# Kernel optimization log

Measured on AMD Instinct MI355X. Metric: run time of the kernel, lower is better.

Reference implementation:

```python
import jax, jax.numpy as jnp
import numpy as np

T, B, D, H, L = 64, 512, 1536, 1024, 4
DISCOUNT = 0.997
LAM = 0.95


def setup_inputs() -> dict:
    key = jax.random.key(0)
    ks = jax.random.split(key, 3 + L + 1)
    inp = {
        'feat': jax.random.normal(ks[0], (T, B, D), dtype=jnp.float32),
        'reward': jax.random.normal(ks[1], (T - 1, B), dtype=jnp.float32),
        'cont': jnp.ones((T, B), dtype=jnp.float32),
    }
    scale = 0.02
    dims = [D] + [H] * L
    for i in range(L):
        inp[f'W{i}'] = jax.random.normal(ks[3 + i], (dims[i], dims[i + 1]), dtype=jnp.float32) * scale
        inp[f'b{i}'] = jnp.zeros((dims[i + 1],), dtype=jnp.float32)
    inp['Wo'] = jax.random.normal(ks[3 + L], (H,), dtype=jnp.float32) * scale
    inp['bo'] = jnp.zeros((), dtype=jnp.float32)
    return inp


def reference(feat, reward, cont, W0, b0, W1, b1, W2, b2, W3, b3, Wo, bo):
    # Value-net MLP (mean of critic dist): [T, B, D] -> [T, B]
    h = feat
    for W, b in ((W0, b0), (W1, b1), (W2, b2), (W3, b3)):
        h = jax.nn.silu(h @ W + b)
    value = h @ Wo + bo  # [T, B]

    disc = cont[1:] * DISCOUNT                      # [T-1, B]
    deltas = reward + disc * value[1:] - value[:-1]  # [T-1, B]

    # GAE: adv_t = delta_t + disc_t * lambda * adv_{t+1}, adv_T = 0
    def step(adv_next, xs):
        delta, dl = xs
        adv = delta + dl * adv_next
        return adv, adv

    _, advs = jax.lax.scan(step, jnp.zeros_like(value[0]),
                           (deltas, disc * LAM), reverse=True)
    ret = advs + value[:-1]   # lambda-return target, [T-1, B]
    baseline = value[:-1]
    return ret, baseline
```

## Files before the change

kernel.cpp:

```cpp
#include <hip/hip_runtime.h>
#include <hip/hip_bf16.h>

#define T_DIM 64
#define B_DIM 512
#define D_DIM 1536
#define H_DIM 1024
#define M_DIM (T_DIM * B_DIM)
#define DISCOUNT 0.997f
#define LAM 0.95f

#define BM 128
#define BN 128
#define BK 64
#define TILES_M 256
#define TILES_N 8
#define N_XCD 8

typedef __bf16 bf16x8 __attribute__((ext_vector_type(8)));
typedef float  f32x4  __attribute__((ext_vector_type(4)));

__device__ __forceinline__ void async_load16(const void* g, void* l) {
    __builtin_amdgcn_global_load_lds(
        (const __attribute__((address_space(1))) void*)g,
        (__attribute__((address_space(3))) void*)l,
        16, 0, 0);
}

__device__ __forceinline__ unsigned short f2bf_raw(float f) {
    __hip_bfloat16 h = __float2bfloat16(f);
    return *reinterpret_cast<unsigned short*>(&h);
}

__global__ __launch_bounds__(256) void cvt_bf16_kernel(
    const float* __restrict__ x, __hip_bfloat16* __restrict__ y, long n4) {
    long i = (long)blockIdx.x * blockDim.x + threadIdx.x;
    if (i >= n4) return;
    float4 v = reinterpret_cast<const float4*>(x)[i];
    ushort4 o;
    o.x = f2bf_raw(v.x);
    o.y = f2bf_raw(v.y);
    o.z = f2bf_raw(v.z);
    o.w = f2bf_raw(v.w);
    reinterpret_cast<ushort4*>(y)[i] = o;
}

__global__ __launch_bounds__(256) void transpose_cvt_all_kernel(
    const float* __restrict__ W0, const float* __restrict__ W1,
    const float* __restrict__ W2, const float* __restrict__ W3,
    __hip_bfloat16* __restrict__ T0, __hip_bfloat16* __restrict__ T1,
    __hip_bfloat16* __restrict__ T2, __hip_bfloat16* __restrict__ T3) {
    __shared__ float tile[32][33];
    int z = blockIdx.z;
    const float* W;
    __hip_bfloat16* Tt;
    int K;
    if (z == 0)      { W = W0; Tt = T0; K = D_DIM; }
    else if (z == 1) { W = W1; Tt = T1; K = H_DIM; }
    else if (z == 2) { W = W2; Tt = T2; K = H_DIM; }
    else             { W = W3; Tt = T3; K = H_DIM; }
    int k0 = blockIdx.x * 32, n0 = blockIdx.y * 32;
    if (k0 >= K) return;
    int tx = threadIdx.x, ty = threadIdx.y;
    #pragma unroll
    for (int r = ty; r < 32; r += 8)
        tile[r][tx] = W[(size_t)(k0 + r) * H_DIM + n0 + tx];
    __syncthreads();
    #pragma unroll
    for (int r = ty; r < 32; r += 8)
        Tt[(size_t)(n0 + r) * K + k0 + tx] = __float2bfloat16(tile[tx][r]);
}

__global__ __launch_bounds__(256) void gemm_silu_kernel(
    const __hip_bfloat16* __restrict__ A,
    const __hip_bfloat16* __restrict__ Bt,
    const float* __restrict__ bias,
    __hip_bfloat16* __restrict__ C,
    int K) {

    __shared__ alignas(16) __hip_bfloat16 As[2][BM * BK];
    __shared__ alignas(16) __hip_bfloat16 Bs[2][BN * BK];

    const int tid  = threadIdx.x;
    const int wave = tid >> 6;
    const int lane = tid & 63;
    const int sub  = lane >> 3;
    const int quad = lane >> 4;
    const int r16  = lane & 15;
    const int wm   = wave & 1;
    const int wn   = wave >> 1;

    const int l     = blockIdx.x;
    const int xcd   = l & (N_XCD - 1);
    const int local = l >> 3;
    const int tn    = local & (TILES_N - 1);
    const int tm    = (xcd << 5) | (local >> 3);
    const int m0 = tm * BM;
    const int n0 = tn * BN;

    const int scol = (((lane & 7) ^ sub) << 3);

    const __hip_bfloat16* ga[4];
    const __hip_bfloat16* gb[4];
    int ldsoff[4];
    #pragma unroll
    for (int i = 0; i < 4; ++i) {
        int chunk = wave * 4 + i;
        ga[i] = A  + (size_t)(m0 + chunk * 8 + sub) * K + scol;
        gb[i] = Bt + (size_t)(n0 + chunk * 8 + sub) * K + scol;
        ldsoff[i] = chunk * 512;
    }

    f32x4 acc[4][4];
    #pragma unroll
    for (int i = 0; i < 4; ++i)
        #pragma unroll
        for (int j = 0; j < 4; ++j)
            acc[i][j] = (f32x4){0.f, 0.f, 0.f, 0.f};

    const int niter = K / BK;

    #pragma unroll
    for (int i = 0; i < 4; ++i) { async_load16(ga[i], &As[0][ldsoff[i]]); ga[i] += BK; }
    #pragma unroll
    for (int i = 0; i < 4; ++i) { async_load16(gb[i], &Bs[0][ldsoff[i]]); gb[i] += BK; }

    int p = 0;
    for (int k = 0; k < niter; ++k) {
        asm volatile("s_waitcnt vmcnt(0)" ::: "memory");
        asm volatile("s_barrier" ::: "memory");

        if (k + 1 < niter) {
            #pragma unroll
            for (int i = 0; i < 4; ++i) { async_load16(ga[i], &As[p ^ 1][ldsoff[i]]); ga[i] += BK; }
            #pragma unroll
            for (int i = 0; i < 4; ++i) { async_load16(gb[i], &Bs[p ^ 1][ldsoff[i]]); gb[i] += BK; }
        }

        #pragma unroll
        for (int kk = 0; kk < BK; kk += 32) {
            bf16x8 af[4], bf[4];
            #pragma unroll
            for (int i = 0; i < 4; ++i) {
                int m_l = wm * 64 + i * 16 + r16;
                int sa  = ((kk >> 3) + quad) ^ (m_l & 7);
                af[i] = *reinterpret_cast<const bf16x8*>(&As[p][m_l * BK + sa * 8]);
                int n_l = wn * 64 + i * 16 + r16;
                int sb  = ((kk >> 3) + quad) ^ (n_l & 7);
                bf[i] = *reinterpret_cast<const bf16x8*>(&Bs[p][n_l * BK + sb * 8]);
            }
            #pragma unroll
            for (int i = 0; i < 4; ++i)
                #pragma unroll
                for (int j = 0; j < 4; ++j)
                    acc[i][j] = __builtin_amdgcn_mfma_f32_16x16x32_bf16(
                        af[i], bf[j], acc[i][j], 0, 0, 0);
        }
        p ^= 1;
    }

    #pragma unroll
    for (int j = 0; j < 4; ++j) {
        int col = n0 + wn * 64 + j * 16 + r16;
        float bj = bias[col];
        #pragma unroll
        for (int i = 0; i < 4; ++i) {
            int row_base = m0 + wm * 64 + i * 16 + quad * 4;
            #pragma unroll
            for (int rr = 0; rr < 4; ++rr) {
                float v = acc[i][j][rr] + bj;
                float s = v / (1.f + __expf(-v));
                C[(size_t)(row_base + rr) * H_DIM + col] = __float2bfloat16(s);
            }
        }
    }
}

__global__ __launch_bounds__(256) void gemv_value_kernel(
    const __hip_bfloat16* __restrict__ H,
    const float* __restrict__ Wo,
    const float* __restrict__ bo_p,
    float* __restrict__ value, int M) {
    int wave = threadIdx.x >> 6, lane = threadIdx.x & 63;
    int row = blockIdx.x * 4 + wave;
    if (row >= M) return;
    const __hip_bfloat16* hrow = H + (size_t)row * H_DIM;
    float sum = 0.f;
    #pragma unroll
    for (int half = 0; half < 2; ++half) {
        int col = half * 512 + lane * 8;
        uint4 raw = *reinterpret_cast<const uint4*>(hrow + col);
        const __hip_bfloat16* hp = reinterpret_cast<const __hip_bfloat16*>(&raw);
        #pragma unroll
        for (int e = 0; e < 8; ++e)
            sum += __bfloat162float(hp[e]) * Wo[col + e];
    }
    #pragma unroll
    for (int off = 32; off > 0; off >>= 1)
        sum += __shfl_down(sum, off, 64);
    if (lane == 0) value[row] = sum + bo_p[0];
}

__global__ __launch_bounds__(64) void gae_kernel(
    const float* __restrict__ value,
    const float* __restrict__ reward,
    const float* __restrict__ cont,
    float* __restrict__ out) {
    int b = blockIdx.x * blockDim.x + threadIdx.x;
    if (b >= B_DIM) return;
    float adv = 0.f;
    float v_next = value[(T_DIM - 1) * B_DIM + b];
    for (int t = T_DIM - 2; t >= 0; --t) {
        float v_t  = value[t * B_DIM + b];
        float disc = cont[(t + 1) * B_DIM + b] * DISCOUNT;
        float delta = reward[t * B_DIM + b] + disc * v_next - v_t;
        adv = delta + disc * LAM * adv;
        out[t * B_DIM + b] = adv + v_t;
        out[(T_DIM - 1) * B_DIM + t * B_DIM + b] = v_t;
        v_next = v_t;
    }
}

extern "C" void kernel_launch(void* const* d_in, const int* in_sizes, int n_in,
                              void* d_out, int out_size, void* d_ws, size_t ws_size,
                              hipStream_t stream) {
    const float* feat   = (const float*)d_in[0];
    const float* reward = (const float*)d_in[1];
    const float* cont   = (const float*)d_in[2];
    const float* W[4]   = {(const float*)d_in[3], (const float*)d_in[5],
                           (const float*)d_in[7], (const float*)d_in[9]};
    const float* bias[4] = {(const float*)d_in[4], (const float*)d_in[6],
                            (const float*)d_in[8], (const float*)d_in[10]};
    const float* Wo = (const float*)d_in[11];
    const float* bo = (const float*)d_in[12];
    float* out = (float*)d_out;

    char* ws = (char*)d_ws;
    __hip_bfloat16* Xb = (__hip_bfloat16*)ws; ws += (size_t)M_DIM * D_DIM * 2;
    __hip_bfloat16* Ha = (__hip_bfloat16*)ws; ws += (size_t)M_DIM * H_DIM * 2;
    __hip_bfloat16* Hb = (__hip_bfloat16*)ws; ws += (size_t)M_DIM * H_DIM * 2;
    __hip_bfloat16* Wt0 = (__hip_bfloat16*)ws; ws += (size_t)H_DIM * D_DIM * 2;
    __hip_bfloat16* Wt1 = (__hip_bfloat16*)ws; ws += (size_t)H_DIM * H_DIM * 2;
    __hip_bfloat16* Wt2 = (__hip_bfloat16*)ws; ws += (size_t)H_DIM * H_DIM * 2;
    __hip_bfloat16* Wt3 = (__hip_bfloat16*)ws; ws += (size_t)H_DIM * H_DIM * 2;
    float* value = (float*)ws; ws += (size_t)M_DIM * 4;

    long n4 = (long)M_DIM * D_DIM / 4;
    cvt_bf16_kernel<<<(int)((n4 + 255) / 256), 256, 0, stream>>>(feat, Xb, n4);

    transpose_cvt_all_kernel<<<dim3(D_DIM / 32, H_DIM / 32, 4), dim3(32, 8), 0, stream>>>(
        W[0], W[1], W[2], W[3], Wt0, Wt1, Wt2, Wt3);

    const int nblocks = TILES_M * TILES_N;
    gemm_silu_kernel<<<nblocks, 256, 0, stream>>>(Xb, Wt0, bias[0], Ha, D_DIM);
    gemm_silu_kernel<<<nblocks, 256, 0, stream>>>(Ha, Wt1, bias[1], Hb, H_DIM);
    gemm_silu_kernel<<<nblocks, 256, 0, stream>>>(Hb, Wt2, bias[2], Ha, H_DIM);
    gemm_silu_kernel<<<nblocks, 256, 0, stream>>>(Ha, Wt3, bias[3], Hb, H_DIM);

    gemv_value_kernel<<<M_DIM / 4, 256, 0, stream>>>(Hb, Wo, bo, value, M_DIM);

    gae_kernel<<<8, 64, 0, stream>>>(value, reward, cont, out);
}
```

Measured before the change: 758.3 us.

## Enlarge GEMM tiles to 256x256 and fuse value GEMV into last layer

Each GEMM block now computes a 256x256 tile with 512 threads, using dynamic LDS for the double-buffered A/B tiles. Each wave holds an 8x4 grid of MFMA accumulators, which raises operand reuse per LDS read and halves global re-reads of A and B. The final layer skips writing its activation and instead reduces silu(h)·Wo per row. It uses shuffles plus atomicAdd into a value buffer that is zeroed beforehand, and the bias bo is added later in the GAE kernel. The trade-offs: 128KB of LDS per block limits residency to one block per CU, and the float atomics make the summation order nondeterministic.

```diff
diff --git a/kernel.cpp b/kernel.cpp
--- a/kernel.cpp
+++ b/kernel.cpp
@@ -9,12 +9,13 @@
 #define DISCOUNT 0.997f
 #define LAM 0.95f
 
-#define BM 128
-#define BN 128
+#define BM 256
+#define BN 256
 #define BK 64
-#define TILES_M 256
-#define TILES_N 8
+#define TILES_M 128
+#define TILES_N 4
 #define N_XCD 8
+#define GEMM_LDS_BYTES (2 * (BM + BN) * BK * 2)
 
 typedef __bf16 bf16x8 __attribute__((ext_vector_type(8)));
 typedef float  f32x4  __attribute__((ext_vector_type(4)));
@@ -70,15 +71,18 @@
         Tt[(size_t)(n0 + r) * K + k0 + tx] = __float2bfloat16(tile[tx][r]);
 }
 
-__global__ __launch_bounds__(256) void gemm_silu_kernel(
+__global__ __launch_bounds__(512, 2) void gemm_silu_kernel(
     const __hip_bfloat16* __restrict__ A,
     const __hip_bfloat16* __restrict__ Bt,
     const float* __restrict__ bias,
     __hip_bfloat16* __restrict__ C,
+    const float* __restrict__ Wo,
+    float* __restrict__ value,
     int K) {
 
-    __shared__ alignas(16) __hip_bfloat16 As[2][BM * BK];
-    __shared__ alignas(16) __hip_bfloat16 Bs[2][BN * BK];
+    extern __shared__ __align__(16) __hip_bfloat16 smem[];
+    __hip_bfloat16* AsBuf = smem;
+    __hip_bfloat16* BsBuf = smem + 2 * BM * BK;
 
     const int tid  = threadIdx.x;
     const int wave = tid >> 6;
@@ -93,7 +97,7 @@
     const int xcd   = l & (N_XCD - 1);
     const int local = l >> 3;
     const int tn    = local & (TILES_N - 1);
-    const int tm    = (xcd << 5) | (local >> 3);
+    const int tm    = (xcd << 4) | (local >> 2);
     const int m0 = tm * BM;
     const int n0 = tn * BN;
 
@@ -101,18 +105,16 @@
 
     const __hip_bfloat16* ga[4];
     const __hip_bfloat16* gb[4];
-    int ldsoff[4];
     #pragma unroll
     for (int i = 0; i < 4; ++i) {
         int chunk = wave * 4 + i;
         ga[i] = A  + (size_t)(m0 + chunk * 8 + sub) * K + scol;
         gb[i] = Bt + (size_t)(n0 + chunk * 8 + sub) * K + scol;
-        ldsoff[i] = chunk * 512;
-    }
-
-    f32x4 acc[4][4];
-    #pragma unroll
-    for (int i = 0; i < 4; ++i)
+    }
+
+    f32x4 acc[8][4];
+    #pragma unroll
+    for (int i = 0; i < 8; ++i)
         #pragma unroll
         for (int j = 0; j < 4; ++j)
             acc[i][j] = (f32x4){0.f, 0.f, 0.f, 0.f};
@@ -120,9 +122,10 @@
     const int niter = K / BK;
 
     #pragma unroll
-    for (int i = 0; i < 4; ++i) { async_load16(ga[i], &As[0][ldsoff[i]]); ga[i] += BK; }
-    #pragma unroll
-    for (int i = 0; i < 4; ++i) { async_load16(gb[i], &Bs[0][ldsoff[i]]); gb[i] += BK; }
+    for (int i = 0; i < 4; ++i) {
+        async_load16(ga[i], &AsBuf[(wave * 4 + i) * 512]); ga[i] += BK;
+        async_load16(gb[i], &BsBuf[(wave * 4 + i) * 512]); gb[i] += BK;
+    }
 
     int p = 0;
     for (int k = 0; k < niter; ++k) {
@@ -130,87 +133,97 @@
         asm volatile("s_barrier" ::: "memory");
 
         if (k + 1 < niter) {
-            #pragma unroll
-            for (int i = 0; i < 4; ++i) { async_load16(ga[i], &As[p ^ 1][ldsoff[i]]); ga[i] += BK; }
-            #pragma unroll
-            for (int i = 0; i < 4; ++i) { async_load16(gb[i], &Bs[p ^ 1][ldsoff[i]]); gb[i] += BK; }
-        }
-
+            int q = p ^ 1;
+            #pragma unroll
+            for (int i = 0; i < 4; ++i) {
+                async_load16(ga[i], &AsBuf[q * (BM * BK) + (wave * 4 + i) * 512]); ga[i] += BK;
+                async_load16(gb[i], &BsBuf[q * (BM * BK) + (wave * 4 + i) * 512]); gb[i] += BK;
+            }
+        }
+
+        const __hip_bfloat16* As = &AsBuf[p * (BM * BK)];
+        const __hip_bfloat16* Bs = &BsBuf[p * (BM * BK)];
         #pragma unroll
         for (int kk = 0; kk < BK; kk += 32) {
-            bf16x8 af[4], bf[4];
-            #pragma unroll
-            for (int i = 0; i < 4; ++i) {
-                int m_l = wm * 64 + i * 16 + r16;
+            bf16x8 bf[4];
+            #pragma unroll
+            for (int j = 0; j < 4; ++j) {
+                int n_l = wn * 64 + j * 16 + r16;
+                int sb  = ((kk >> 3) + quad) ^ (n_l & 7);
+                bf[j] = *reinterpret_cast<const bf16x8*>(&Bs[n_l * BK + sb * 8]);
+            }
+            #pragma unroll
+            for (int i = 0; i < 8; ++i) {
+                int m_l = wm * 128 + i * 16 + r16;
                 int sa  = ((kk >> 3) + quad) ^ (m_l & 7);
-                af[i] = *reinterpret_cast<const bf16x8*>(&As[p][m_l * BK + sa * 8]);
-                int n_l = wn * 64 + i * 16 + r16;
-                int sb  = ((kk >> 3) + quad) ^ (n_l & 7);
-                bf[i] = *reinterpret_cast<const bf16x8*>(&Bs[p][n_l * BK + sb * 8]);
-            }
-            #pragma unroll
-            for (int i = 0; i < 4; ++i)
+                bf16x8 af = *reinterpret_cast<const bf16x8*>(&As[m_l * BK + sa * 8]);
                 #pragma unroll
                 for (int j = 0; j < 4; ++j)
                     acc[i][j] = __builtin_amdgcn_mfma_f32_16x16x32_bf16(
-                        af[i], bf[j], acc[i][j], 0, 0, 0);
+                        af, bf[j], acc[i][j], 0, 0, 0);
+            }
         }
         p ^= 1;
     }
+
+    const bool do_c = (C != nullptr);
+    const bool do_v = (Wo != nullptr);
+    float rowsum[8][4];
+    #pragma unroll
+    for (int i = 0; i < 8; ++i)
+        #pragma unroll
+        for (int rr = 0; rr < 4; ++rr) rowsum[i][rr] = 0.f;
 
     #pragma unroll
     for (int j = 0; j < 4; ++j) {
         int col = n0 + wn * 64 + j * 16 + r16;
         float bj = bias[col];
-        #pragma unroll
-        for (int i = 0; i < 4; ++i) {
-            int row_base = m0 + wm * 64 + i * 16 + quad * 4;
+        float wj = do_v ? Wo[col] : 0.f;
+        #pragma unroll
+        for (int i = 0; i < 8; ++i) {
+            int row_base = m0 + wm * 128 + i * 16 + quad * 4;
             #pragma unroll
             for (int rr = 0; rr < 4; ++rr) {
                 float v = acc[i][j][rr] + bj;
                 float s = v / (1.f + __expf(-v));
-                C[(size_t)(row_base + rr) * H_DIM + col] = __float2bfloat16(s);
-            }
-        }
-    }
-}
-
-__global__ __launch_bounds__(256) void gemv_value_kernel(
-    const __hip_bfloat16* __restrict__ H,
-    const float* __restrict__ Wo,
-    const float* __restrict__ bo_p,
-    float* __restrict__ value, int M) {
-    int wave = threadIdx.x >> 6, lane = threadIdx.x & 63;
-    int row = blockIdx.x * 4 + wave;
-    if (row >= M) return;
-    const __hip_bfloat16* hrow = H + (size_t)row * H_DIM;
-    float sum = 0.f;
-    #pragma unroll
-    for (int half = 0; half < 2; ++half) {
-        int col = half * 512 + lane * 8;
-        uint4 raw = *reinterpret_cast<const uint4*>(hrow + col);
-        const __hip_bfloat16* hp = reinterpret_cast<const __hip_bfloat16*>(&raw);
-        #pragma unroll
-        for (int e = 0; e < 8; ++e)
-            sum += __bfloat162float(hp[e]) * Wo[col + e];
-    }
-    #pragma unroll
-    for (int off = 32; off > 0; off >>= 1)
-        sum += __shfl_down(sum, off, 64);
-    if (lane == 0) value[row] = sum + bo_p[0];
+                if (do_c)
+                    C[(size_t)(row_base + rr) * H_DIM + col] = __float2bfloat16(s);
+                rowsum[i][rr] += s * wj;
+            }
+        }
+    }
+    if (do_v) {
+        #pragma unroll
+        for (int i = 0; i < 8; ++i) {
+            #pragma unroll
+            for (int rr = 0; rr < 4; ++rr) {
+                float rs = rowsum[i][rr];
+                rs += __shfl_xor(rs, 1, 64);
+                rs += __shfl_xor(rs, 2, 64);
+                rs += __shfl_xor(rs, 4, 64);
+                rs += __shfl_xor(rs, 8, 64);
+                if (r16 == 0) {
+                    int row = m0 + wm * 128 + i * 16 + quad * 4 + rr;
+                    atomicAdd(&value[row], rs);
+                }
+            }
+        }
+    }
 }
 
 __global__ __launch_bounds__(64) void gae_kernel(
     const float* __restrict__ value,
     const float* __restrict__ reward,
     const float* __restrict__ cont,
+    const float* __restrict__ bo_p,
     float* __restrict__ out) {
     int b = blockIdx.x * blockDim.x + threadIdx.x;
     if (b >= B_DIM) return;
+    float bo = bo_p[0];
     float adv = 0.f;
-    float v_next = value[(T_DIM - 1) * B_DIM + b];
+    float v_next = value[(T_DIM - 1) * B_DIM + b] + bo;
     for (int t = T_DIM - 2; t >= 0; --t) {
-        float v_t  = value[t * B_DIM + b];
+        float v_t  = value[t * B_DIM + b] + bo;
         float disc = cont[(t + 1) * B_DIM + b] * DISCOUNT;
         float delta = reward[t * B_DIM + b] + disc * v_next - v_t;
         adv = delta + disc * LAM * adv;
@@ -244,19 +257,27 @@
     __hip_bfloat16* Wt3 = (__hip_bfloat16*)ws; ws += (size_t)H_DIM * H_DIM * 2;
     float* value = (float*)ws; ws += (size_t)M_DIM * 4;
 
+    (void)hipFuncSetAttribute((const void*)gemm_silu_kernel,
+                              hipFuncAttributeMaxDynamicSharedMemorySize,
+                              GEMM_LDS_BYTES);
+
     long n4 = (long)M_DIM * D_DIM / 4;
     cvt_bf16_kernel<<<(int)((n4 + 255) / 256), 256, 0, stream>>>(feat, Xb, n4);
 
     transpose_cvt_all_kernel<<<dim3(D_DIM / 32, H_DIM / 32, 4), dim3(32, 8), 0, stream>>>(
         W[0], W[1], W[2], W[3], Wt0, Wt1, Wt2, Wt3);
 
+    hipMemsetAsync(value, 0, (size_t)M_DIM * 4, stream);
+
     const int nblocks = TILES_M * TILES_N;
-    gemm_silu_kernel<<<nblocks, 256, 0, stream>>>(Xb, Wt0, bias[0], Ha, D_DIM);
-    gemm_silu_kernel<<<nblocks, 256, 0, stream>>>(Ha, Wt1, bias[1], Hb, H_DIM);
-    gemm_silu_kernel<<<nblocks, 256, 0, stream>>>(Hb, Wt2, bias[2], Ha, H_DIM);
-    gemm_silu_kernel<<<nblocks, 256, 0, stream>>>(Ha, Wt3, bias[3], Hb, H_DIM);
-
-    gemv_value_kernel<<<M_DIM / 4, 256, 0, stream>>>(Hb, Wo, bo, value, M_DIM);
-
-    gae_kernel<<<8, 64, 0, stream>>>(value, reward, cont, out);
-}
+    gemm_silu_kernel<<<nblocks, 512, GEMM_LDS_BYTES, stream>>>(
+        Xb, Wt0, bias[0], Ha, nullptr, nullptr, D_DIM);
+    gemm_silu_kernel<<<nblocks, 512, GEMM_LDS_BYTES, stream>>>(
+        Ha, Wt1, bias[1], Hb, nullptr, nullptr, H_DIM);
+    gemm_silu_kernel<<<nblocks, 512, GEMM_LDS_BYTES, stream>>>(
+        Hb, Wt2, bias[2], Ha, nullptr, nullptr, H_DIM);
+    gemm_silu_kernel<<<nblocks, 512, GEMM_LDS_BYTES, stream>>>(
+        Ha, Wt3, bias[3], nullptr, Wo, value, H_DIM);
+
+    gae_kernel<<<8, 64, 0, stream>>>(value, reward, cont, bo, out);
+}
```

Measured after the change: 722.5 us. 1.05x faster.
